# Performance work log

Hardware: AMD Instinct MI355X
Metric: run time of the kernel (lower is better)

Reference implementation:

```python
import jax, jax.numpy as jnp
import numpy as np
import math

B, L, D, H = 2, 2048, 1024, 16
d = D // H

def setup_inputs() -> dict:
    key = jax.random.key(0)
    ks = jax.random.split(key, 12)
    s = 0.02
    return {
        "x": jax.random.normal(ks[0], (B, L, D), jnp.float32),
        "Wqkv_w": jax.random.normal(ks[1], (D, 3 * D), jnp.float32) * s,
        "Wqkv_b": jax.random.normal(ks[2], (3 * D,), jnp.float32) * s,
        "out_w": jax.random.normal(ks[3], (D, D), jnp.float32) * s,
        "out_b": jax.random.normal(ks[4], (D,), jnp.float32) * s,
        "W_static": jnp.zeros((H, d, d), jnp.float32),
        "Lambda_raw": jax.random.uniform(ks[5], (H, d, d), jnp.float32, -3.0, 3.0),
        "Gamma": jax.random.uniform(ks[6], (H, d, d), jnp.float32, -0.5 / math.sqrt(d), 0.5 / math.sqrt(d)),
        "gate_w1": jax.random.normal(ks[7], (D, D // 2), jnp.float32) * s,
        "gate_b1": jax.random.normal(ks[8], (D // 2,), jnp.float32) * s,
        "gate_w2": jax.random.normal(ks[9], (D // 2, H), jnp.float32) * s,
        "gate_b2": jax.random.normal(ks[10], (H,), jnp.float32) * s,
    }

def _forward(x, Wqkv_w, Wqkv_b, out_w, out_b, W_static, Lambda_raw, Gamma,
             gate_w1, gate_b1, gate_w2, gate_b2):
    scale = 1.0 / math.sqrt(d)
    qkv = x @ Wqkv_w + Wqkv_b                              # (B,L,3D)
    qkv = qkv.reshape(B, L, 3, H, d).transpose(2, 0, 3, 1, 4)  # (3,B,H,L,d)
    q, k, v = qkv[0], qkv[1], qkv[2]

    # --- causal softmax attention branch ---
    scores = jnp.einsum('bhid,bhjd->bhij', q, k) * scale
    mask = jnp.triu(jnp.full((L, L), -10000.0, scores.dtype), 1)
    attn = jax.nn.softmax(scores + mask, axis=-1)
    y_softmax = jnp.einsum('bhij,bhjd->bhid', attn, v)     # (B,H,L,d)

    # --- STP fast-weight branch: decaying Hebbian state recurrence ---
    k_stp = k * scale
    retention = 1.0 - jax.nn.sigmoid(Lambda_raw)           # (H,d,d)
    def step(state, qkv_t):
        q_t, k_t, v_t = qkv_t                              # each (B,H,d)
        hebbian = v_t[..., :, None] * k_t[..., None, :]    # (B,H,d,d)
        state = retention * state + Gamma * hebbian
        y_t = jnp.einsum('bhij,bhj->bhi', W_static + state, q_t)
        return state, y_t
    qkv_seq = (q.transpose(2, 0, 1, 3), k_stp.transpose(2, 0, 1, 3), v.transpose(2, 0, 1, 3))
    state0 = jnp.zeros((B, H, d, d), x.dtype)
    _, y_stp = jax.lax.scan(step, state0, qkv_seq)         # (L,B,H,d)
    y_stp = y_stp.transpose(1, 2, 0, 3)                    # (B,H,L,d)

    # --- learned gate ---
    h = jax.nn.gelu(x @ gate_w1 + gate_b1, approximate=False)
    alpha = jax.nn.sigmoid(h @ gate_w2 + gate_b2)          # (B,L,H)
    alpha = alpha.transpose(0, 2, 1)[..., None]            # (B,H,L,1)

    y = alpha * y_softmax + (1.0 - alpha) * y_stp          # (B,H,L,d)
    y = y.transpose(0, 2, 1, 3).reshape(B, L, D)
    return y @ out_w + out_b

def reference(x, Wqkv_w, Wqkv_b, out_w, out_b, W_static, Lambda_raw, Gamma,
              gate_w1, gate_b1, gate_w2, gate_b2):
    return _forward(x, Wqkv_w, Wqkv_b, out_w, out_b, W_static, Lambda_raw, Gamma,
                    gate_w1, gate_b1, gate_w2, gate_b2)
```

## Files before the change

kernel.cpp:

```cpp
#include <hip/hip_runtime.h>
#include <cstdint>
#include <cstddef>

#define B_ 2
#define L_ 2048
#define D_ 1024
#define H_ 16
#define DH 64

typedef __attribute__((ext_vector_type(8))) short bf16x8;
typedef __attribute__((ext_vector_type(4))) float f32x4;
typedef unsigned short u16;

__device__ inline u16 f2bf(float f) {
  unsigned u = __builtin_bit_cast(unsigned, f);
  u += 0x7fffu + ((u >> 16) & 1u);
  return (u16)(u >> 16);
}

__device__ inline float bf2f(u16 x) {
  return __builtin_bit_cast(float, (unsigned)x << 16);
}

template <int CTRL>
__device__ inline float dpp_mov(float x) {
  int t = __builtin_amdgcn_update_dpp(0, __builtin_bit_cast(int, x), CTRL, 0xf, 0xf, true);
  return __builtin_bit_cast(float, t);
}

#define GLDS16(ldst, gsrc)                                              \
  __builtin_amdgcn_global_load_lds(                                    \
      (const __attribute__((address_space(1))) void*)(gsrc),           \
      (__attribute__((address_space(3))) void*)(ldst), 16, 0, 0)

__device__ inline void stp_upd(float4& z, const float4 r, const float4 g,
                               const float4 wlc, float vv,
                               float kx, float ky, float kz, float kw) {
  z.x = fmaf(r.x, z.x, fmaf(g.x * vv, kx, wlc.x));
  z.y = fmaf(r.y, z.y, fmaf(g.y * vv, ky, wlc.y));
  z.z = fmaf(r.z, z.z, fmaf(g.z * vv, kz, wlc.z));
  z.w = fmaf(r.w, z.w, fmaf(g.w * vv, kw, wlc.w));
}

__device__ inline void stp_upd1(float4& z, const float4 r, const float4 g,
                                float vv, float kx, float ky, float kz, float kw) {
  z.x = fmaf(r.x, z.x, (g.x * vv) * kx);
  z.y = fmaf(r.y, z.y, (g.y * vv) * ky);
  z.z = fmaf(r.z, z.z, (g.z * vv) * kz);
  z.w = fmaf(r.w, z.w, (g.w * vv) * kw);
}

__device__ inline float stp_dot(const float4 z, float qx, float qy, float qz, float qw) {
  float p = z.x * qx;
  p = fmaf(z.y, qy, p);
  p = fmaf(z.z, qz, p);
  p = fmaf(z.w, qw, p);
  return p;
}

__device__ inline float dpp_red16(float p) {
  p = p + dpp_mov<0x128>(p);
  p = p + dpp_mov<0x124>(p);
  p = p + dpp_mov<0x122>(p);
  p = p + dpp_mov<0x121>(p);
  return p;
}


__device__ inline void d_transpose(const float* __restrict__ in,
                                   u16* __restrict__ out, int R, int C,
                                   int bx, int by, float tile[32][33], int tid) {
  const int tx = tid & 31, ty = tid >> 5;
  const int c0 = bx * 32, r0 = by * 32;
#pragma unroll
  for (int j = 0; j < 4; ++j)
    tile[ty + j * 8][tx] = in[(size_t)(r0 + ty + j * 8) * C + c0 + tx];
  __syncthreads();
#pragma unroll
  for (int j = 0; j < 4; ++j)
    out[(size_t)(c0 + ty + j * 8) * R + r0 + tx] = f2bf(tile[tx][ty + j * 8]);
}

__global__ __launch_bounds__(256) void prep_fused(
    const float* __restrict__ x, u16* __restrict__ xbf,
    const float* __restrict__ wqkv_w, u16* __restrict__ wqkvT,
    const float* __restrict__ out_w, u16* __restrict__ owT,
    const float* __restrict__ g_w1, u16* __restrict__ g1T,
    const float* __restrict__ lam, const float* __restrict__ gma,
    float* __restrict__ retb, float* __restrict__ gamb,
    float* __restrict__ retb64) {
  __shared__ float tile[32][33];
  const int bid = blockIdx.x, tid = threadIdx.x;
  if (bid < 4096) {
    int i = bid * 256 + tid;
    float4 v = ((const float4*)x)[i];
    ushort4 o;
    o.x = f2bf(v.x); o.y = f2bf(v.y); o.z = f2bf(v.z); o.w = f2bf(v.w);
    ((ushort4*)xbf)[i] = o;
  } else if (bid < 7168) {
    int r = bid - 4096;
    d_transpose(wqkv_w, wqkvT, 1024, 3072, r % 96, r / 96, tile, tid);
  } else if (bid < 8192) {
    int r = bid - 7168;
    d_transpose(out_w, owT, 1024, 1024, r % 32, r / 32, tile, tid);
  } else if (bid < 8704) {
    int r = bid - 8192;
    d_transpose(g_w1, g1T, 1024, 512, r % 16, r / 16, tile, tid);
  } else {
    int i = (bid - 8704) * 256 + tid;
    float l = lam[i];
    float r = 1.f / (1.f + expf(l));
    retb[i] = r;
    gamb[i] = gma[i] * 0.125f;
    float r2 = r * r;
    float r4 = r2 * r2;
    float r8 = r4 * r4;
    float r16 = r8 * r8;
    float r32 = r16 * r16;
    retb64[i] = r32 * r32;
  }
}


struct GemmP {
  const u16* A; const u16* Bt; int M, N, K;
  const float* bias;
  u16* qb; u16* kb; u16* vtb;
  float* hout;
  float* outp;
};

template <int EPI>
__global__ __launch_bounds__(256, 2) void gemm_kernel(GemmP p) {
  __shared__ u16 As[128 * 32];
  __shared__ u16 Bs[128 * 32];
  __shared__ u16 tileT[EPI == 0 ? 128 * 136 : 1];
  const int tid = threadIdx.x;
  const int lane = tid & 63;
  const int w = tid >> 6;
  const int wr = w >> 1, wc = w & 1;
  const int lr = lane & 15, lk = lane >> 4;
  const int nwgx = gridDim.x;
  int lin = blockIdx.x + nwgx * blockIdx.y;
  const int cpx = (nwgx * gridDim.y) >> 3;
  lin = (lin & 7) * cpx + (lin >> 3);
  const int m0 = (lin / nwgx) * 128, n0 = (lin % nwgx) * 128;

  f32x4 acc[4][4];
#pragma unroll
  for (int i = 0; i < 4; ++i)
#pragma unroll
    for (int j = 0; j < 4; ++j) acc[i][j] = (f32x4){0.f, 0.f, 0.f, 0.f};

  for (int k0 = 0; k0 < p.K; k0 += 32) {
    __syncthreads();
#pragma unroll
    for (int it = 0; it < 2; ++it) {
      int idx = it * 256 + tid;
      int row = idx >> 2, ch = idx & 3;
      GLDS16(&As[idx * 8], p.A + (size_t)(m0 + row) * p.K + k0 + ch * 8);
      GLDS16(&Bs[idx * 8], p.Bt + (size_t)(n0 + row) * p.K + k0 + ch * 8);
    }
    __syncthreads();
    bf16x8 af[4], bfr[4];
#pragma unroll
    for (int mr = 0; mr < 4; ++mr)
      af[mr] = *(const bf16x8*)&As[(wr * 64 + mr * 16 + lr) * 32 + lk * 8];
#pragma unroll
    for (int nr = 0; nr < 4; ++nr)
      bfr[nr] = *(const bf16x8*)&Bs[(wc * 64 + nr * 16 + lr) * 32 + lk * 8];
#pragma unroll
    for (int mr = 0; mr < 4; ++mr)
#pragma unroll
      for (int nr = 0; nr < 4; ++nr)
        acc[mr][nr] = __builtin_amdgcn_mfma_f32_16x16x32_bf16(af[mr], bfr[nr], acc[mr][nr], 0, 0, 0);
  }

  if constexpr (EPI == 0) {
    if (n0 < 2048) {
#pragma unroll
      for (int mr = 0; mr < 4; ++mr)
#pragma unroll
        for (int nr = 0; nr < 4; ++nr) {
          const int col = n0 + wc * 64 + nr * 16 + lr;
#pragma unroll
          for (int rr = 0; rr < 4; ++rr) {
            const int row = m0 + wr * 64 + mr * 16 + lk * 4 + rr;
            float v = acc[mr][nr][rr] + p.bias[col];
            int which = col >> 10, hh = (col >> 6) & 15, ii = col & 63;
            int b = row >> 11, ll = row & 2047;
            size_t bi = ((size_t)(b * 16 + hh) * L_ + ll) * 64 + ii;
            if (which == 0) p.qb[bi] = f2bf(v * 0.125f);
            else            p.kb[bi] = f2bf(v);
          }
        }
    } else {
#pragma unroll
      for (int mr = 0; mr < 4; ++mr)
#pragma unroll
        for (int nr = 0; nr < 4; ++nr) {
          const int cl = wc * 64 + nr * 16 + lr;
          const float bv = p.bias[n0 + cl];
#pragma unroll
          for (int rr = 0; rr < 4; ++rr) {
            const int rl = wr * 64 + mr * 16 + lk * 4 + rr;
            tileT[cl * 136 + rl] = f2bf(acc[mr][nr][rr] + bv);
          }
        }
      __syncthreads();
      const int c = tid >> 1, h = tid & 1;
      const int vcol = (n0 - 2048) + c;
      const int hh = vcol >> 6, ii = vcol & 63;
      const int b = m0 >> 11;
      const int ll0 = (m0 & 2047) + h * 64;
      u16* dst = p.vtb + ((size_t)(b * 16 + hh) * 64 + ii) * L_ + ll0;
      const u16* src = &tileT[c * 136 + h * 64];
#pragma unroll
      for (int k = 0; k < 8; ++k)
        *(int4*)(dst + k * 8) = *(const int4*)(src + k * 8);
    }
  } else {
#pragma unroll
    for (int mr = 0; mr < 4; ++mr)
#pragma unroll
      for (int nr = 0; nr < 4; ++nr) {
        const int col = n0 + wc * 64 + nr * 16 + lr;
#pragma unroll
        for (int rr = 0; rr < 4; ++rr) {
          const int row = m0 + wr * 64 + mr * 16 + lk * 4 + rr;
          float v = acc[mr][nr][rr] + p.bias[col];
          if constexpr (EPI == 1) {
            float g = 0.5f * v * (1.f + erff(v * 0.70710678118f));
            p.hout[(size_t)row * p.N + col] = g;
          } else {
            p.outp[(size_t)row * p.N + col] = v;
          }
        }
      }
  }
}


__global__ __launch_bounds__(256) void alpha_kernel(
    const float* __restrict__ hbuf, const float* __restrict__ w2,
    const float* __restrict__ b2, float* __restrict__ alp) {
  const int tid = threadIdx.x;
  const int row = blockIdx.x * 16 + (tid >> 4);
  const int n = tid & 15;
  const float4* h4 = (const float4*)(hbuf + (size_t)row * 512);
  float acc = 0.f;
#pragma unroll 2
  for (int kk = 0; kk < 128; ++kk) {
    float4 hv = h4[kk];
    acc = fmaf(hv.x, w2[(kk * 4 + 0) * 16 + n], acc);
    acc = fmaf(hv.y, w2[(kk * 4 + 1) * 16 + n], acc);
    acc = fmaf(hv.z, w2[(kk * 4 + 2) * 16 + n], acc);
    acc = fmaf(hv.w, w2[(kk * 4 + 3) * 16 + n], acc);
  }
  float z = acc + b2[n];
  alp[row * 16 + n] = 1.f / (1.f + __expf(-z));
}


__global__ __launch_bounds__(256, 2) void attn_kernel(
    const u16* __restrict__ qb, const u16* __restrict__ kb,
    const u16* __restrict__ vtb, float* __restrict__ ysm) {
  __shared__ u16 Ks[64 * 64];
  __shared__ u16 Vts[64 * 64];
  __shared__ u16 Pl[4][16 * 64];
  const int tid = threadIdx.x, lane = tid & 63, w = tid >> 6;
  const int lr = lane & 15, lk = lane >> 4;
  const int lin = (int)blockIdx.x + 16 * (int)blockIdx.y;
  const int bh = lin & 31;
  const int xp = lin >> 5;
  const int qtA = 31 - xp, qtB = xp;

  const u16* kbase0 = kb + (size_t)bh * (L_ * 64);
  const u16* vbase0 = vtb + (size_t)bh * (64 * L_);

  const size_t qbaseA = ((size_t)bh * L_ + qtA * 64 + w * 16 + lr) * 64;
  const size_t qbaseB = ((size_t)bh * L_ + qtB * 64 + w * 16 + lr) * 64;
  bf16x8 qfrA[2], qfrB[2];
  qfrA[0] = *(const bf16x8*)(qb + qbaseA + lk * 8);
  qfrA[1] = *(const bf16x8*)(qb + qbaseA + 32 + lk * 8);
  qfrB[0] = *(const bf16x8*)(qb + qbaseB + lk * 8);
  qfrB[1] = *(const bf16x8*)(qb + qbaseB + 32 + lk * 8);

  f32x4 yaccA[4], yaccB[4];
  float mrowA[4], lrowA[4], mrowB[4], lrowB[4];
#pragma unroll
  for (int i = 0; i < 4; ++i) {
    yaccA[i] = (f32x4){0.f, 0.f, 0.f, 0.f};
    yaccB[i] = (f32x4){0.f, 0.f, 0.f, 0.f};
    mrowA[i] = -1e30f; mrowB[i] = -1e30f;
    lrowA[i] = 0.f;    lrowB[i] = 0.f;
  }

  auto process = [&](const bf16x8* qfr, f32x4* yacc, float* mrow, float* lrow,
                     bool maskTile) {
    f32x4 s[4];
#pragma unroll
    for (int f = 0; f < 4; ++f) {
      f32x4 sf = (f32x4){0.f, 0.f, 0.f, 0.f};
#pragma unroll
      for (int ss = 0; ss < 2; ++ss) {
        bf16x8 kfr = *(const bf16x8*)&Ks[(f * 16 + lr) * 64 +
                                         (((ss * 4 + lk) ^ (lr & 7)) * 8)];
        sf = __builtin_amdgcn_mfma_f32_16x16x32_bf16(qfr[ss], kfr, sf, 0, 0, 0);
      }
      s[f] = sf;
    }
    if (maskTile) {
#pragma unroll
      for (int f = 0; f < 4; ++f)
#pragma unroll
        for (int rr = 0; rr < 4; ++rr)
          if (f * 16 + lr > w * 16 + lk * 4 + rr) s[f][rr] = -1e30f;
    }
    float mx[4];
#pragma unroll
    for (int rr = 0; rr < 4; ++rr) {
      float m = fmaxf(fmaxf(s[0][rr], s[1][rr]), fmaxf(s[2][rr], s[3][rr]));
      m = fmaxf(m, dpp_mov<0x128>(m));
      m = fmaxf(m, dpp_mov<0x124>(m));
      m = fmaxf(m, dpp_mov<0x122>(m));
      m = fmaxf(m, dpp_mov<0x121>(m));
      mx[rr] = m;
    }
    bool need = (mx[0] > mrow[0] + 8.f) | (mx[1] > mrow[1] + 8.f) |
                (mx[2] > mrow[2] + 8.f) | (mx[3] > mrow[3] + 8.f);
    if (__any(need)) {
#pragma unroll
      for (int rr = 0; rr < 4; ++rr) {
        float mn = fmaxf(mrow[rr], mx[rr]);
        float c = __expf(mrow[rr] - mn);
        lrow[rr] *= c;
#pragma unroll
        for (int nf = 0; nf < 4; ++nf) yacc[nf][rr] *= c;
        mrow[rr] = mn;
      }
    }
    u16* pw = &Pl[w][0];
#pragma unroll
    for (int rr = 0; rr < 4; ++rr) {
      const int prow = lk * 4 + rr;
      float rs = 0.f;
#pragma unroll
      for (int f = 0; f < 4; ++f) {
        float pv = __expf(s[f][rr] - mrow[rr]);
        rs += pv;
        int chunk = f * 2 + (lr >> 3);
        pw[prow * 64 + ((chunk ^ (prow & 7)) * 8) + (lr & 7)] = f2bf(pv);
      }
      rs = rs + dpp_mov<0x128>(rs);
      rs = rs + dpp_mov<0x124>(rs);
      rs = rs + dpp_mov<0x122>(rs);
      rs = rs + dpp_mov<0x121>(rs);
      lrow[rr] += rs;
    }
#pragma unroll
    for (int s2 = 0; s2 < 2; ++s2) {
      bf16x8 pa = *(const bf16x8*)&pw[lr * 64 + (((s2 * 4 + lk) ^ (lr & 7)) * 8)];
#pragma unroll
      for (int nf = 0; nf < 4; ++nf) {
        bf16x8 vfr = *(const bf16x8*)&Vts[(nf * 16 + lr) * 64 +
                                          (((s2 * 4 + lk) ^ (lr & 7)) * 8)];
        yacc[nf] = __builtin_amdgcn_mfma_f32_16x16x32_bf16(pa, vfr, yacc[nf], 0, 0, 0);
      }
    }
  };

  const int nkv = qtA + 1;
  for (int kt = 0; kt < nkv; ++kt) {
    const int kv0 = kt * 64;
    __syncthreads();
#pragma unroll
    for (int it = 0; it < 2; ++it) {
      int idx = it * 256 + tid;
      int row = idx >> 3, ch = idx & 7;
      int sch = (ch ^ (row & 7)) * 8;
      *(int4*)&Ks[row * 64 + sch] =
          *(const int4*)(kbase0 + (size_t)(kv0 + row) * 64 + ch * 8);
      *(int4*)&Vts[row * 64 + sch] =
          *(const int4*)(vbase0 + (size_t)row * L_ + kv0 + ch * 8);
    }
    __syncthreads();

    process(qfrA, yaccA, mrowA, lrowA, kt == qtA);
    if (kt <= qtB) process(qfrB, yaccB, mrowB, lrowB, kt == qtB);
  }

#pragma unroll
  for (int nf = 0; nf < 4; ++nf)
#pragma unroll
    for (int rr = 0; rr < 4; ++rr) {
      int rowl = w * 16 + lk * 4 + rr;
      int col = nf * 16 + lr;
      ysm[((size_t)bh * L_ + qtA * 64 + rowl) * 64 + col] = yaccA[nf][rr] / lrowA[rr];
      ysm[((size_t)bh * L_ + qtB * 64 + rowl) * 64 + col] = yaccB[nf][rr] / lrowB[rr];
    }
}


__global__ __launch_bounds__(256, 4) void stp_pass1(
    const u16* __restrict__ kb, const u16* __restrict__ vtb,
    const float* __restrict__ retb, const float* __restrict__ gamb,
    float* __restrict__ slocal) {
  __shared__ u16 Klds[4096];
  const int tid = threadIdx.x, lane = tid & 63, w = tid >> 6;
  const int bh = blockIdx.x >> 5, c = blockIdx.x & 31;
  const int hh = bh & 15;
  const int m = lane >> 4, j4 = (lane & 15) * 4;
  const int i0m = w * 16 + m * 4;

  const u16* kcb = kb + ((size_t)bh * L_ + c * 64) * 64;
  GLDS16(&Klds[tid * 8], kcb + tid * 8);
  GLDS16(&Klds[2048 + tid * 8], kcb + 2048 + tid * 8);
  __syncthreads();

  const int hij = (hh * 64 + i0m) * 64 + j4;
  const float4 r0 = *(const float4*)(retb + hij);
  const float4 r1 = *(const float4*)(retb + hij + 64);
  const float4 r2 = *(const float4*)(retb + hij + 128);
  const float4 r3 = *(const float4*)(retb + hij + 192);
  const float4 g0 = *(const float4*)(gamb + hij);
  const float4 g1 = *(const float4*)(gamb + hij + 64);
  const float4 g2 = *(const float4*)(gamb + hij + 128);
  const float4 g3 = *(const float4*)(gamb + hij + 192);
  const u16* vbp = vtb + ((size_t)bh * 64 + i0m) * L_ + c * 64;

  float4 s0 = {0,0,0,0}, s1 = {0,0,0,0}, s2 = {0,0,0,0}, s3 = {0,0,0,0};
#pragma unroll 1
  for (int t8 = 0; t8 < 8; ++t8) {
    const bf16x8 va = *(const bf16x8*)(vbp + t8 * 8);
    const bf16x8 vb = *(const bf16x8*)(vbp + L_ + t8 * 8);
    const bf16x8 vc = *(const bf16x8*)(vbp + 2 * L_ + t8 * 8);
    const bf16x8 vd = *(const bf16x8*)(vbp + 3 * L_ + t8 * 8);
#pragma unroll
    for (int tt = 0; tt < 8; ++tt) {
      const ushort4 k4u = *(const ushort4*)&Klds[(t8 * 8 + tt) * 64 + j4];
      const float kx = bf2f(k4u.x), ky = bf2f(k4u.y),
                  kz = bf2f(k4u.z), kw = bf2f(k4u.w);
      stp_upd1(s0, r0, g0, bf2f((u16)va[tt]), kx, ky, kz, kw);
      stp_upd1(s1, r1, g1, bf2f((u16)vb[tt]), kx, ky, kz, kw);
      stp_upd1(s2, r2, g2, bf2f((u16)vc[tt]), kx, ky, kz, kw);
      stp_upd1(s3, r3, g3, bf2f((u16)vd[tt]), kx, ky, kz, kw);
    }
  }
  float* sb = slocal + (((size_t)(bh * 32 + c) * 64) + i0m) * 64 + j4;
  *(float4*)(sb)       = s0;
  *(float4*)(sb + 64)  = s1;
  *(float4*)(sb + 128) = s2;
  *(float4*)(sb + 192) = s3;
}

__global__ __launch_bounds__(256) void stp_scan(
    const float* __restrict__ retb64, float* __restrict__ slocal) {
  const int idx = blockIdx.x * 256 + threadIdx.x;
  const int j = idx & 63, i1 = (idx >> 6) & 63, bh = idx >> 12;
  const int hh = bh & 15;
  const float r64 = retb64[(hh * 64 + i1) * 64 + j];
  float carry = 0.f;
  for (int c = 0; c < 32; ++c) {
    const size_t off = ((((size_t)bh * 32 + c) * 64 + i1) * 64 + j);
    const float sl = slocal[off];
    slocal[off] = carry;
    carry = fmaf(r64, carry, sl);
  }
}

__global__ __launch_bounds__(256, 4) void stp_pass2(
    const u16* __restrict__ qb, const u16* __restrict__ kb,
    const u16* __restrict__ vtb, const float* __restrict__ retb,
    const float* __restrict__ gamb, const float* __restrict__ wst,
    const float* __restrict__ slocal, float* __restrict__ ystp) {
  __shared__ u16 KQ[8192];
  const int tid = threadIdx.x, lane = tid & 63, w = tid >> 6;
  const int bh = blockIdx.x >> 5, c = blockIdx.x & 31;
  const int hh = bh & 15;
  const int m = lane >> 4, jc = lane & 15, j4 = jc * 4;
  const int i0m = w * 16 + m * 4;

  const size_t cb = ((size_t)bh * L_ + c * 64) * 64;
  GLDS16(&KQ[tid * 8], kb + cb + tid * 8);
  GLDS16(&KQ[2048 + tid * 8], kb + cb + 2048 + tid * 8);
  GLDS16(&KQ[4096 + tid * 8], qb + cb + tid * 8);
  GLDS16(&KQ[6144 + tid * 8], qb + cb + 2048 + tid * 8);
  __syncthreads();

  const int hij = (hh * 64 + i0m) * 64 + j4;
  const float4 r0 = *(const float4*)(retb + hij);
  const float4 r1 = *(const float4*)(retb + hij + 64);
  const float4 r2 = *(const float4*)(retb + hij + 128);
  const float4 r3 = *(const float4*)(retb + hij + 192);
  const float4 g0 = *(const float4*)(gamb + hij);
  const float4 g1 = *(const float4*)(gamb + hij + 64);
  const float4 g2 = *(const float4*)(gamb + hij + 128);
  const float4 g3 = *(const float4*)(gamb + hij + 192);
  const float4 w0 = *(const float4*)(wst + hij);
  const float4 w1 = *(const float4*)(wst + hij + 64);
  const float4 w2 = *(const float4*)(wst + hij + 128);
  const float4 w3 = *(const float4*)(wst + hij + 192);

  const float* sb = slocal + (((size_t)(bh * 32 + c) * 64) + i0m) * 64 + j4;
  float4 z0 = *(const float4*)(sb);
  float4 z1 = *(const float4*)(sb + 64);
  float4 z2 = *(const float4*)(sb + 128);
  float4 z3 = *(const float4*)(sb + 192);

  float4 wlc0, wlc1, wlc2, wlc3;
  wlc0.x = w0.x * (1.f - r0.x); wlc0.y = w0.y * (1.f - r0.y);
  wlc0.z = w0.z * (1.f - r0.z); wlc0.w = w0.w * (1.f - r0.w);
  wlc1.x = w1.x * (1.f - r1.x); wlc1.y = w1.y * (1.f - r1.y);
  wlc1.z = w1.z * (1.f - r1.z); wlc1.w = w1.w * (1.f - r1.w);
  wlc2.x = w2.x * (1.f - r2.x); wlc2.y = w2.y * (1.f - r2.y);
  wlc2.z = w2.z * (1.f - r2.z); wlc2.w = w2.w * (1.f - r2.w);
  wlc3.x = w3.x * (1.f - r3.x); wlc3.y = w3.y * (1.f - r3.y);
  wlc3.z = w3.z * (1.f - r3.z); wlc3.w = w3.w * (1.f - r3.w);
  z0.x += w0.x; z0.y += w0.y; z0.z += w0.z; z0.w += w0.w;
  z1.x += w1.x; z1.y += w1.y; z1.z += w1.z; z1.w += w1.w;
  z2.x += w2.x; z2.y += w2.y; z2.z += w2.z; z2.w += w2.w;
  z3.x += w3.x; z3.y += w3.y; z3.z += w3.z; z3.w += w3.w;

  const u16* vbp = vtb + ((size_t)bh * 64 + i0m) * L_ + c * 64;
  float* yp = ystp + cb + i0m;

#pragma unroll 1
  for (int t8 = 0; t8 < 8; ++t8) {
    const bf16x8 va = *(const bf16x8*)(vbp + t8 * 8);
    const bf16x8 vb = *(const bf16x8*)(vbp + L_ + t8 * 8);
    const bf16x8 vc = *(const bf16x8*)(vbp + 2 * L_ + t8 * 8);
    const bf16x8 vd = *(const bf16x8*)(vbp + 3 * L_ + t8 * 8);
#pragma unroll
    for (int tt = 0; tt < 8; ++tt) {
      const int t = t8 * 8 + tt;
      const ushort4 k4u = *(const ushort4*)&KQ[t * 64 + j4];
      const ushort4 q4u = *(const ushort4*)&KQ[4096 + t * 64 + j4];
      const float kx = bf2f(k4u.x), ky = bf2f(k4u.y),
                  kz = bf2f(k4u.z), kw = bf2f(k4u.w);
      const float qx = bf2f(q4u.x), qy = bf2f(q4u.y),
                  qz = bf2f(q4u.z), qw = bf2f(q4u.w);
      stp_upd(z0, r0, g0, wlc0, bf2f((u16)va[tt]), kx, ky, kz, kw);
      stp_upd(z1, r1, g1, wlc1, bf2f((u16)vb[tt]), kx, ky, kz, kw);
      stp_upd(z2, r2, g2, wlc2, bf2f((u16)vc[tt]), kx, ky, kz, kw);
      stp_upd(z3, r3, g3, wlc3, bf2f((u16)vd[tt]), kx, ky, kz, kw);
      float p0 = dpp_red16(stp_dot(z0, qx, qy, qz, qw));
      float p1 = dpp_red16(stp_dot(z1, qx, qy, qz, qw));
      float p2 = dpp_red16(stp_dot(z2, qx, qy, qz, qw));
      float p3 = dpp_red16(stp_dot(z3, qx, qy, qz, qw));
      if (jc == 0) {
        float4 yo;
        yo.x = p0 * 8.f; yo.y = p1 * 8.f; yo.z = p2 * 8.f; yo.w = p3 * 8.f;
        *(float4*)(yp + t * 64) = yo;
      }
    }
  }
}


__global__ __launch_bounds__(256) void blend_kernel(
    const float* __restrict__ ysm, const float* __restrict__ ystp,
    const float* __restrict__ alp, u16* __restrict__ ycomb) {
  int idx = blockIdx.x * 256 + threadIdx.x;
  int m = idx >> 8;
  int n4 = (idx & 255) * 4;
  int hh = n4 >> 6, ii = n4 & 63;
  int b = m >> 11, ll = m & 2047;
  size_t bi = ((size_t)(b * 16 + hh) * L_ + ll) * 64 + ii;
  float a = alp[m * 16 + hh];
  float4 s = *(const float4*)(ysm + bi);
  float4 t = *(const float4*)(ystp + bi);
  ushort4 o;
  o.x = f2bf(a * s.x + (1.f - a) * t.x);
  o.y = f2bf(a * s.y + (1.f - a) * t.y);
  o.z = f2bf(a * s.z + (1.f - a) * t.z);
  o.w = f2bf(a * s.w + (1.f - a) * t.w);
  *(ushort4*)(ycomb + (size_t)m * 1024 + n4) = o;
}


extern "C" void kernel_launch(void* const* d_in, const int* in_sizes, int n_in,
                              void* d_out, int out_size, void* d_ws, size_t ws_size,
                              hipStream_t stream) {
  const float* x       = (const float*)d_in[0];
  const float* wqkv_w  = (const float*)d_in[1];
  const float* wqkv_b  = (const float*)d_in[2];
  const float* out_w   = (const float*)d_in[3];
  const float* out_b   = (const float*)d_in[4];
  const float* w_stat  = (const float*)d_in[5];
  const float* lam     = (const float*)d_in[6];
  const float* gma     = (const float*)d_in[7];
  const float* g_w1    = (const float*)d_in[8];
  const float* g_b1    = (const float*)d_in[9];
  const float* g_w2    = (const float*)d_in[10];
  const float* g_b2    = (const float*)d_in[11];

  char* ws = (char*)d_ws;
  size_t off = 0;
  auto nxt = [&](size_t b) { size_t r = off; off += (b + 255) & ~(size_t)255; return r; };
  u16*   xbf   = (u16*)(ws + nxt((size_t)4096 * 1024 * 2));
  u16*   wqkvT = (u16*)(ws + nxt((size_t)3072 * 1024 * 2));
  u16*   owT   = (u16*)(ws + nxt((size_t)1024 * 1024 * 2));
  u16*   g1T   = (u16*)(ws + nxt((size_t)512 * 1024 * 2));
  u16*   qb    = (u16*)(ws + nxt((size_t)4194304 * 2));
  u16*   kb    = (u16*)(ws + nxt((size_t)4194304 * 2));
  u16*   vtb   = (u16*)(ws + nxt((size_t)4194304 * 2));
  float* ysm   = (float*)(ws + nxt((size_t)4194304 * 4));
  float* ystp  = (float*)(ws + nxt((size_t)4194304 * 4));
  size_t hbuf_off = nxt((size_t)4096 * 512 * 4);
  float* hbuf  = (float*)(ws + hbuf_off);
  float* alp   = (float*)(ws + nxt((size_t)4096 * 16 * 4));
  u16*   ycomb = (u16*)(ws + nxt((size_t)4096 * 1024 * 2));
  float* retb  = (float*)(ws + nxt((size_t)65536 * 4));
  float* gamb  = (float*)(ws + nxt((size_t)65536 * 4));
  float* retb64= (float*)(ws + nxt((size_t)65536 * 4));
  float* slocal = (float*)(ws + hbuf_off);

  dim3 blk(256);
  prep_fused<<<8960, blk, 0, stream>>>(x, xbf, wqkv_w, wqkvT, out_w, owT,
                                       g_w1, g1T, lam, gma, retb, gamb, retb64);

  GemmP p0 = {xbf, wqkvT, 4096, 3072, 1024, wqkv_b,
              qb, kb, vtb, nullptr, nullptr};
  gemm_kernel<0><<<dim3(24, 32), blk, 0, stream>>>(p0);

  stp_pass1<<<1024, blk, 0, stream>>>(kb, vtb, retb, gamb, slocal);
  stp_scan<<<512, blk, 0, stream>>>(retb64, slocal);
  stp_pass2<<<1024, blk, 0, stream>>>(qb, kb, vtb, retb, gamb, w_stat, slocal, ystp);

  GemmP p1 = {xbf, g1T, 4096, 512, 1024, g_b1,
              nullptr, nullptr, nullptr, hbuf, nullptr};
  gemm_kernel<1><<<dim3(4, 32), blk, 0, stream>>>(p1);

  alpha_kernel<<<256, blk, 0, stream>>>(hbuf, g_w2, g_b2, alp);

  attn_kernel<<<dim3(16, 32), blk, 0, stream>>>(qb, kb, vtb, ysm);

  blend_kernel<<<4096, blk, 0, stream>>>(ysm, ystp, alp, ycomb);

  GemmP p2 = {ycomb, owT, 4096, 1024, 1024, out_b,
              nullptr, nullptr, nullptr, nullptr, (float*)d_out};
  gemm_kernel<2><<<dim3(8, 32), blk, 0, stream>>>(p2);
}
```

Before: 271.1 us.

## Merge independent kernels into combined launches to fill GPU concurrently

Folds the QKV GEMM and the gate GEMM into one launch, with blocks picking their job by index, and folds the attention kernel and STP pass1 into one launch sharing an LDS buffer. The aim is to cut launch gaps and tail underutilisation by letting independent work run side by side on the CUs. To make this safe, the workspace is rearranged so slocal (which aliases hbuf) is only written after alpha has consumed hbuf. The cost is that the combined kernels take the larger LDS footprint and launch bounds, which may lower occupancy for the lighter branch: stp_pass1 goes from a bound of 4 to 2.

```diff
diff --git a/kernel.cpp b/kernel.cpp
--- a/kernel.cpp
+++ b/kernel.cpp
@@ -131,19 +131,15 @@
 };
 
 template <int EPI>
-__global__ __launch_bounds__(256, 2) void gemm_kernel(GemmP p) {
-  __shared__ u16 As[128 * 32];
-  __shared__ u16 Bs[128 * 32];
-  __shared__ u16 tileT[EPI == 0 ? 128 * 136 : 1];
+__device__ void gemm_body(const GemmP& p, int lin0, int nwgx, int nwgtot,
+                          u16* As, u16* Bs, u16* tileT) {
   const int tid = threadIdx.x;
   const int lane = tid & 63;
   const int w = tid >> 6;
   const int wr = w >> 1, wc = w & 1;
   const int lr = lane & 15, lk = lane >> 4;
-  const int nwgx = gridDim.x;
-  int lin = blockIdx.x + nwgx * blockIdx.y;
-  const int cpx = (nwgx * gridDim.y) >> 3;
-  lin = (lin & 7) * cpx + (lin >> 3);
+  const int cpx = nwgtot >> 3;
+  const int lin = (lin0 & 7) * cpx + (lin0 >> 3);
   const int m0 = (lin / nwgx) * 128, n0 = (lin % nwgx) * 128;
 
   f32x4 acc[4][4];
@@ -238,6 +234,22 @@
         }
       }
   }
+}
+
+__global__ __launch_bounds__(256, 2) void gemm01_kernel(GemmP p0, GemmP p1) {
+  __shared__ u16 As[128 * 32];
+  __shared__ u16 Bs[128 * 32];
+  __shared__ u16 tileT[128 * 136];
+  const int bid = blockIdx.x;
+  if (bid < 768) gemm_body<0>(p0, bid, 24, 768, As, Bs, tileT);
+  else           gemm_body<1>(p1, bid - 768, 4, 128, As, Bs, tileT);
+}
+
+__global__ __launch_bounds__(256, 2) void gemm2_kernel(GemmP p) {
+  __shared__ u16 As[128 * 32];
+  __shared__ u16 Bs[128 * 32];
+  const int lin0 = (int)blockIdx.x + 8 * (int)blockIdx.y;
+  gemm_body<2>(p, lin0, 8, 256, As, Bs, nullptr);
 }
 
 
@@ -262,15 +274,14 @@
 }
 
 
-__global__ __launch_bounds__(256, 2) void attn_kernel(
-    const u16* __restrict__ qb, const u16* __restrict__ kb,
-    const u16* __restrict__ vtb, float* __restrict__ ysm) {
-  __shared__ u16 Ks[64 * 64];
-  __shared__ u16 Vts[64 * 64];
-  __shared__ u16 Pl[4][16 * 64];
+__device__ void attn_body(int lin, u16* sbuf,
+                          const u16* __restrict__ qb, const u16* __restrict__ kb,
+                          const u16* __restrict__ vtb, float* __restrict__ ysm) {
+  u16* Ks = sbuf;
+  u16* Vts = sbuf + 4096;
+  u16* Pl = sbuf + 8192;
   const int tid = threadIdx.x, lane = tid & 63, w = tid >> 6;
   const int lr = lane & 15, lk = lane >> 4;
-  const int lin = (int)blockIdx.x + 16 * (int)blockIdx.y;
   const int bh = lin & 31;
   const int xp = lin >> 5;
   const int qtA = 31 - xp, qtB = xp;
@@ -340,7 +351,7 @@
         mrow[rr] = mn;
       }
     }
-    u16* pw = &Pl[w][0];
+    u16* pw = Pl + w * 1024;
 #pragma unroll
     for (int rr = 0; rr < 4; ++rr) {
       const int prow = lk * 4 + rr;
@@ -402,13 +413,13 @@
 }
 
 
-__global__ __launch_bounds__(256, 4) void stp_pass1(
-    const u16* __restrict__ kb, const u16* __restrict__ vtb,
-    const float* __restrict__ retb, const float* __restrict__ gamb,
-    float* __restrict__ slocal) {
-  __shared__ u16 Klds[4096];
+__device__ void stp1_body(int bid, u16* Klds,
+                          const u16* __restrict__ kb, const u16* __restrict__ vtb,
+                          const float* __restrict__ retb,
+                          const float* __restrict__ gamb,
+                          float* __restrict__ slocal) {
   const int tid = threadIdx.x, lane = tid & 63, w = tid >> 6;
-  const int bh = blockIdx.x >> 5, c = blockIdx.x & 31;
+  const int bh = bid >> 5, c = bid & 31;
   const int hh = bh & 15;
   const int m = lane >> 4, j4 = (lane & 15) * 4;
   const int i0m = w * 16 + m * 4;
@@ -452,6 +463,17 @@
   *(float4*)(sb + 64)  = s1;
   *(float4*)(sb + 128) = s2;
   *(float4*)(sb + 192) = s3;
+}
+
+__global__ __launch_bounds__(256, 2) void attn_stp1_kernel(
+    const u16* __restrict__ qb, const u16* __restrict__ kb,
+    const u16* __restrict__ vtb, float* __restrict__ ysm,
+    const float* __restrict__ retb, const float* __restrict__ gamb,
+    float* __restrict__ slocal) {
+  __shared__ u16 sbuf[12288];
+  const int bid = blockIdx.x;
+  if (bid < 512) attn_body(bid, sbuf, qb, kb, vtb, ysm);
+  else           stp1_body(bid - 512, sbuf, kb, vtb, retb, gamb, slocal);
 }
 
 __global__ __launch_bounds__(256) void stp_scan(
@@ -609,12 +631,12 @@
   float* ystp  = (float*)(ws + nxt((size_t)4194304 * 4));
   size_t hbuf_off = nxt((size_t)4096 * 512 * 4);
   float* hbuf  = (float*)(ws + hbuf_off);
+  u16*   ycomb = (u16*)(ws + nxt((size_t)4096 * 1024 * 2));
+  float* slocal = (float*)(ws + hbuf_off);
   float* alp   = (float*)(ws + nxt((size_t)4096 * 16 * 4));
-  u16*   ycomb = (u16*)(ws + nxt((size_t)4096 * 1024 * 2));
   float* retb  = (float*)(ws + nxt((size_t)65536 * 4));
   float* gamb  = (float*)(ws + nxt((size_t)65536 * 4));
   float* retb64= (float*)(ws + nxt((size_t)65536 * 4));
-  float* slocal = (float*)(ws + hbuf_off);
 
   dim3 blk(256);
   prep_fused<<<8960, blk, 0, stream>>>(x, xbf, wqkv_w, wqkvT, out_w, owT,
@@ -622,23 +644,22 @@
 
   GemmP p0 = {xbf, wqkvT, 4096, 3072, 1024, wqkv_b,
               qb, kb, vtb, nullptr, nullptr};
-  gemm_kernel<0><<<dim3(24, 32), blk, 0, stream>>>(p0);
-
-  stp_pass1<<<1024, blk, 0, stream>>>(kb, vtb, retb, gamb, slocal);
-  stp_scan<<<512, blk, 0, stream>>>(retb64, slocal);
-  stp_pass2<<<1024, blk, 0, stream>>>(qb, kb, vtb, retb, gamb, w_stat, slocal, ystp);
-
   GemmP p1 = {xbf, g1T, 4096, 512, 1024, g_b1,
               nullptr, nullptr, nullptr, hbuf, nullptr};
-  gemm_kernel<1><<<dim3(4, 32), blk, 0, stream>>>(p1);
+  gemm01_kernel<<<896, blk, 0, stream>>>(p0, p1);
 
   alpha_kernel<<<256, blk, 0, stream>>>(hbuf, g_w2, g_b2, alp);
 
-  attn_kernel<<<dim3(16, 32), blk, 0, stream>>>(qb, kb, vtb, ysm);
+  attn_stp1_kernel<<<1536, blk, 0, stream>>>(qb, kb, vtb, ysm,
+                                             retb, gamb, slocal);
+
+  stp_scan<<<512, blk, 0, stream>>>(retb64, slocal);
+  stp_pass2<<<1024, blk, 0, stream>>>(qb, kb, vtb, retb, gamb, w_stat,
+                                      slocal, ystp);
 
   blend_kernel<<<4096, blk, 0, stream>>>(ysm, ystp, alp, ycomb);
 
   GemmP p2 = {ycomb, owT, 4096, 1024, 1024, out_b,
               nullptr, nullptr, nullptr, nullptr, (float*)d_out};
-  gemm_kernel<2><<<dim3(8, 32), blk, 0, stream>>>(p2);
-}
+  gemm2_kernel<<<dim3(8, 32), blk, 0, stream>>>(p2);
+}
```

After: 252.8 us. 1.07x faster.

## Merge QKV and gate GEMMs into one launch and swizzle GEMM LDS layout

Applied to the files above, without the earlier changes.

Runs the QKV projection GEMM and the gate first-layer GEMM in a single grid of 896 workgroups, removing one launch and giving the small gate GEMM's tiles to CUs that would otherwise sit idle. It also XOR-swizzles the 16-byte chunk index in the A/B LDS tiles to cut bank conflicts on fragment reads. Kernels are reordered so alpha and attention run before the STP passes, and the workspace is rearranged so slocal, which aliases hbuf, is only written after alpha has consumed hbuf. The combined kernel reserves the large transpose tile in LDS for every block, which may lower occupancy for the gate part.

```diff
diff --git a/kernel.cpp b/kernel.cpp
--- a/kernel.cpp
+++ b/kernel.cpp
@@ -131,20 +131,18 @@
 };
 
 template <int EPI>
-__global__ __launch_bounds__(256, 2) void gemm_kernel(GemmP p) {
-  __shared__ u16 As[128 * 32];
-  __shared__ u16 Bs[128 * 32];
-  __shared__ u16 tileT[EPI == 0 ? 128 * 136 : 1];
+__device__ void gemm_body(const GemmP& p, int lin0, int nwgx, int nwgtot,
+                          u16* As, u16* Bs, u16* tileT) {
   const int tid = threadIdx.x;
   const int lane = tid & 63;
   const int w = tid >> 6;
   const int wr = w >> 1, wc = w & 1;
   const int lr = lane & 15, lk = lane >> 4;
-  const int nwgx = gridDim.x;
-  int lin = blockIdx.x + nwgx * blockIdx.y;
-  const int cpx = (nwgx * gridDim.y) >> 3;
-  lin = (lin & 7) * cpx + (lin >> 3);
+  const int cpx = nwgtot >> 3;
+  const int lin = (lin0 & 7) * cpx + (lin0 >> 3);
   const int m0 = (lin / nwgx) * 128, n0 = (lin % nwgx) * 128;
+
+  const int csw = lk ^ ((lr >> 1) & 3);
 
   f32x4 acc[4][4];
 #pragma unroll
@@ -157,7 +155,8 @@
 #pragma unroll
     for (int it = 0; it < 2; ++it) {
       int idx = it * 256 + tid;
-      int row = idx >> 2, ch = idx & 3;
+      int row = idx >> 2;
+      int ch = (idx & 3) ^ ((idx >> 3) & 3);
       GLDS16(&As[idx * 8], p.A + (size_t)(m0 + row) * p.K + k0 + ch * 8);
       GLDS16(&Bs[idx * 8], p.Bt + (size_t)(n0 + row) * p.K + k0 + ch * 8);
     }
@@ -165,10 +164,10 @@
     bf16x8 af[4], bfr[4];
 #pragma unroll
     for (int mr = 0; mr < 4; ++mr)
-      af[mr] = *(const bf16x8*)&As[(wr * 64 + mr * 16 + lr) * 32 + lk * 8];
+      af[mr] = *(const bf16x8*)&As[(wr * 64 + mr * 16 + lr) * 32 + csw * 8];
 #pragma unroll
     for (int nr = 0; nr < 4; ++nr)
-      bfr[nr] = *(const bf16x8*)&Bs[(wc * 64 + nr * 16 + lr) * 32 + lk * 8];
+      bfr[nr] = *(const bf16x8*)&Bs[(wc * 64 + nr * 16 + lr) * 32 + csw * 8];
 #pragma unroll
     for (int mr = 0; mr < 4; ++mr)
 #pragma unroll
@@ -238,6 +237,22 @@
         }
       }
   }
+}
+
+__global__ __launch_bounds__(256, 2) void gemm01_kernel(GemmP p0, GemmP p1) {
+  __shared__ u16 As[128 * 32];
+  __shared__ u16 Bs[128 * 32];
+  __shared__ u16 tileT[128 * 136];
+  const int bid = blockIdx.x;
+  if (bid < 768) gemm_body<0>(p0, bid, 24, 768, As, Bs, tileT);
+  else           gemm_body<1>(p1, bid - 768, 4, 128, As, Bs, tileT);
+}
+
+__global__ __launch_bounds__(256, 2) void gemm2_kernel(GemmP p) {
+  __shared__ u16 As[128 * 32];
+  __shared__ u16 Bs[128 * 32];
+  const int lin0 = (int)blockIdx.x + 8 * (int)blockIdx.y;
+  gemm_body<2>(p, lin0, 8, 256, As, Bs, nullptr);
 }
 
 
@@ -609,12 +624,12 @@
   float* ystp  = (float*)(ws + nxt((size_t)4194304 * 4));
   size_t hbuf_off = nxt((size_t)4096 * 512 * 4);
   float* hbuf  = (float*)(ws + hbuf_off);
+  u16*   ycomb = (u16*)(ws + nxt((size_t)4096 * 1024 * 2));
+  float* slocal = (float*)(ws + hbuf_off);
   float* alp   = (float*)(ws + nxt((size_t)4096 * 16 * 4));
-  u16*   ycomb = (u16*)(ws + nxt((size_t)4096 * 1024 * 2));
   float* retb  = (float*)(ws + nxt((size_t)65536 * 4));
   float* gamb  = (float*)(ws + nxt((size_t)65536 * 4));
   float* retb64= (float*)(ws + nxt((size_t)65536 * 4));
-  float* slocal = (float*)(ws + hbuf_off);
 
   dim3 blk(256);
   prep_fused<<<8960, blk, 0, stream>>>(x, xbf, wqkv_w, wqkvT, out_w, owT,
@@ -622,23 +637,22 @@
 
   GemmP p0 = {xbf, wqkvT, 4096, 3072, 1024, wqkv_b,
               qb, kb, vtb, nullptr, nullptr};
-  gemm_kernel<0><<<dim3(24, 32), blk, 0, stream>>>(p0);
+  GemmP p1 = {xbf, g1T, 4096, 512, 1024, g_b1,
+              nullptr, nullptr, nullptr, hbuf, nullptr};
+  gemm01_kernel<<<896, blk, 0, stream>>>(p0, p1);
+
+  alpha_kernel<<<256, blk, 0, stream>>>(hbuf, g_w2, g_b2, alp);
+
+  attn_kernel<<<dim3(16, 32), blk, 0, stream>>>(qb, kb, vtb, ysm);
 
   stp_pass1<<<1024, blk, 0, stream>>>(kb, vtb, retb, gamb, slocal);
   stp_scan<<<512, blk, 0, stream>>>(retb64, slocal);
-  stp_pass2<<<1024, blk, 0, stream>>>(qb, kb, vtb, retb, gamb, w_stat, slocal, ystp);
-
-  GemmP p1 = {xbf, g1T, 4096, 512, 1024, g_b1,
-              nullptr, nullptr, nullptr, hbuf, nullptr};
-  gemm_kernel<1><<<dim3(4, 32), blk, 0, stream>>>(p1);
-
-  alpha_kernel<<<256, blk, 0, stream>>>(hbuf, g_w2, g_b2, alp);
-
-  attn_kernel<<<dim3(16, 32), blk, 0, stream>>>(qb, kb, vtb, ysm);
+  stp_pass2<<<1024, blk, 0, stream>>>(qb, kb, vtb, retb, gamb, w_stat,
+                                      slocal, ystp);
 
   blend_kernel<<<4096, blk, 0, stream>>>(ysm, ystp, alp, ycomb);
 
   GemmP p2 = {ycomb, owT, 4096, 1024, 1024, out_b,
               nullptr, nullptr, nullptr, nullptr, (float*)d_out};
-  gemm_kernel<2><<<dim3(8, 32), blk, 0, stream>>>(p2);
-}
+  gemm2_kernel<<<dim3(8, 32), blk, 0, stream>>>(p2);
+}
```

Result: faster. 263.3 us (-2.9%).
